# Optimization experiments

Measured on AMD Instinct MI355X. Metric: run time of the kernel, lower is better.

## Reference

```python
import jax, jax.numpy as jnp
import numpy as np

N_HEADS, D_K, D_MODEL = 16, 64, 1024
B, S = 2, 2048


def setup_inputs() -> dict:
    key = jax.random.key(0)
    ks = jax.random.split(key, 9)
    scale = 1.0 / np.sqrt(D_MODEL)
    cscale = 1.0 / np.sqrt(N_HEADS * D_K)
    return {
        "x": jax.random.normal(ks[0], (B, S, D_MODEL), dtype=jnp.float32),
        # per-head projection weights, stacked over heads: [H, d_model, d_k]
        "Wq": jax.random.uniform(ks[1], (N_HEADS, D_MODEL, D_K), jnp.float32, -scale, scale),
        "bq": jax.random.uniform(ks[2], (N_HEADS, D_K), jnp.float32, -scale, scale),
        "Wk": jax.random.uniform(ks[3], (N_HEADS, D_MODEL, D_K), jnp.float32, -scale, scale),
        "bk": jax.random.uniform(ks[4], (N_HEADS, D_K), jnp.float32, -scale, scale),
        "Wv": jax.random.uniform(ks[5], (N_HEADS, D_MODEL, D_K), jnp.float32, -scale, scale),
        "bv": jax.random.uniform(ks[6], (N_HEADS, D_K), jnp.float32, -scale, scale),
        # concat projection: [H*d_k, d_model]
        "Wc": jax.random.uniform(ks[7], (N_HEADS * D_K, D_MODEL), jnp.float32, -cscale, cscale),
        "bc": jax.random.uniform(ks[8], (D_MODEL,), jnp.float32, -cscale, cscale),
    }


def reference(x, Wq, bq, Wk, bk, Wv, bv, Wc, bc):
    # Per-head projections, vectorized across heads: [B,H,S,d_k]
    q = jnp.einsum("bsd,hdk->bhsk", x, Wq) + bq[None, :, None, :]
    k = jnp.einsum("bsd,hdk->bhsk", x, Wk) + bk[None, :, None, :]
    v = jnp.einsum("bsd,hdk->bhsk", x, Wv) + bv[None, :, None, :]
    # scores: [B,H,Sq,Skv]
    scores = jnp.einsum("bhsk,bhtk->bhst", q, k) / jnp.sqrt(jnp.asarray(D_K, x.dtype))
    # FAITHFUL to original: softmax over dim=1 of [B,S,S] = the QUERY axis (axis 2 here)
    attn = jax.nn.softmax(scores, axis=2)
    out = jnp.einsum("bhst,bhtk->bhsk", attn, v)  # [B,H,S,d_k]
    # concat heads along feature dim: [B,S,H*d_k]
    cat = jnp.transpose(out, (0, 2, 1, 3)).reshape(x.shape[0], x.shape[1], -1)
    return cat @ Wc + bc
```

## Files before the change

### kernel.cpp

```cpp
#include <hip/hip_runtime.h>

#define NH 16
#define DK 64
#define DM 1024
#define BB 2
#define SS 2048
#define BS (BB*SS)

typedef __attribute__((ext_vector_type(8))) short bf16x8;
typedef __attribute__((ext_vector_type(4))) short short4v;
typedef __attribute__((ext_vector_type(4))) float f32x4;

#define MFMA16 __builtin_amdgcn_mfma_f32_16x16x32_bf16

static __device__ __forceinline__ float bf2f(short s) {
  union { unsigned u; float f; } v;
  v.u = ((unsigned)(unsigned short)s) << 16;
  return v.f;
}
static __device__ __forceinline__ short f2bf(float f) {
  union { float f; unsigned u; } v; v.f = f;
  unsigned r = (v.u + 0x7fffu + ((v.u >> 16) & 1u)) >> 16;
  return (short)r;
}

template<int C16>
static __device__ __forceinline__ int soff(int row, int chunk) {
  return row*(C16*8) + ((chunk ^ (row & (C16-1))) << 3);
}

template<int C16, int R>
static __device__ __forceinline__ void stage(const short* __restrict__ g, int gstride,
                                             short* l, int wave, int lane) {
  const int rloc = lane / C16;
  const int c    = lane % C16;
#pragma unroll
  for (int rr = 0; rr < R; rr += 4*(64/C16)) {
    int rbase = rr + wave*(64/C16);
    int row   = rbase + rloc;
    int cg    = c ^ (row & (C16-1));
    __builtin_amdgcn_global_load_lds(
        (const __attribute__((address_space(1))) void*)(g + (size_t)row*gstride + cg*8),
        (__attribute__((address_space(3))) void*)(l + rbase*(C16*8)),
        16, 0, 0);
  }
}

__global__ __launch_bounds__(256) void k_convert(
    const float* __restrict__ x,
    const float* __restrict__ Wq, const float* __restrict__ Wk,
    const float* __restrict__ Wv, const float* __restrict__ Wc,
    short* __restrict__ xb, short* __restrict__ Wt, short* __restrict__ Wct) {
  __shared__ float T[64][65];
  const int tid = threadIdx.x;
  int bx = blockIdx.x;
  const int XB = BS*DM/(256*4);
  if (bx < XB) {
    int i = (bx*256 + tid)*4;
    float4 v = *(const float4*)&x[i];
    short4v o; o[0]=f2bf(v.x); o[1]=f2bf(v.y); o[2]=f2bf(v.z); o[3]=f2bf(v.w);
    *(short4v*)&xb[i] = o;
    return;
  }
  bx -= XB;
  if (bx < 48*16) {
    int th = bx >> 4, d0 = (bx & 15) * 64;
    int type = th >> 4, h = th & 15;
    const float* W = ((type == 0) ? Wq : (type == 1) ? Wk : Wv)
                     + (size_t)h*DM*DK + (size_t)d0*DK;
#pragma unroll
    for (int p = 0; p < 4; p++) {
      int dr = p*16 + (tid >> 4), dkc = (tid & 15) * 4;
      float4 v = *(const float4*)&W[(size_t)dr*DK + dkc];
      T[dkc+0][dr]=v.x; T[dkc+1][dr]=v.y; T[dkc+2][dr]=v.z; T[dkc+3][dr]=v.w;
    }
    __syncthreads();
#pragma unroll
    for (int e = 0; e < 2; e++) {
      int c = tid*2 + e, dk = c >> 3, dd = (c & 7) * 8;
      union { short s[8]; int4 v; } u;
#pragma unroll
      for (int j = 0; j < 8; j++) u.s[j] = f2bf(T[dk][dd+j]);
      *(int4*)&Wt[((size_t)th*DK + dk)*DM + d0 + dd] = u.v;
    }
    return;
  }
  bx -= 48*16;
  int n0 = (bx >> 4) * 64, k0 = (bx & 15) * 64;
#pragma unroll
  for (int p = 0; p < 4; p++) {
    int kr = p*16 + (tid >> 4), nc = (tid & 15) * 4;
    float4 v = *(const float4*)&Wc[(size_t)(k0+kr)*DM + n0 + nc];
    T[nc+0][kr]=v.x; T[nc+1][kr]=v.y; T[nc+2][kr]=v.z; T[nc+3][kr]=v.w;
  }
  __syncthreads();
#pragma unroll
  for (int e = 0; e < 2; e++) {
    int c = tid*2 + e, n = c >> 3, kk = (c & 7) * 8;
    union { short s[8]; int4 v; } u;
#pragma unroll
    for (int j = 0; j < 8; j++) u.s[j] = f2bf(T[n][kk+j]);
    *(int4*)&Wct[(size_t)(n0+n)*DM + k0 + kk] = u.v;
  }
}

__global__ __launch_bounds__(256) void k_qkv(
    const short* __restrict__ xb, const short* __restrict__ Wt,
    const float* __restrict__ bq, const float* __restrict__ bk,
    const float* __restrict__ bv,
    short* __restrict__ Qb, short* __restrict__ Kb, short* __restrict__ Vb) {
  __shared__ __align__(16) short As[128*64];
  __shared__ __align__(16) short Bs[128*64];
  const int tid = threadIdx.x, wave = tid >> 6, lane = tid & 63;
  const int l15 = lane & 15, quad = lane >> 4;
  const int m0 = blockIdx.x * 128, n0 = blockIdx.y * 128;
  const int mw = (wave & 1) * 64, nw = (wave >> 1) * 64;
  f32x4 acc[4][4] = {};
  for (int k0 = 0; k0 < DM; k0 += 64) {
    stage<8,128>(xb + (size_t)m0*DM + k0, DM, As, wave, lane);
    stage<8,128>(Wt + (size_t)n0*DM + k0, DM, Bs, wave, lane);
    __syncthreads();
#pragma unroll
    for (int ks = 0; ks < 2; ks++) {
      bf16x8 a[4], b[4];
#pragma unroll
      for (int g = 0; g < 4; g++)  a[g]  = *(const bf16x8*)&As[soff<8>(mw + g*16 + l15,  ks*4 + quad)];
#pragma unroll
      for (int nf = 0; nf < 4; nf++) b[nf] = *(const bf16x8*)&Bs[soff<8>(nw + nf*16 + l15, ks*4 + quad)];
#pragma unroll
      for (int g = 0; g < 4; g++)
#pragma unroll
        for (int nf = 0; nf < 4; nf++)
          acc[g][nf] = MFMA16(a[g], b[nf], acc[g][nf], 0, 0, 0);
    }
    __syncthreads();
  }
  const int th = (n0 + nw) >> 6;
  const int type = th >> 4, h = th & 15;
  short* dst = (type == 0) ? Qb : (type == 1) ? Kb : Vb;
  const float* bias = ((type == 0) ? bq : (type == 1) ? bk : bv) + h*DK;
  const float scale = (type == 0) ? 0.125f : 1.0f;
#pragma unroll
  for (int nf = 0; nf < 4; nf++) {
    int dk = nf*16 + l15;
    float bval = bias[dk];
#pragma unroll
    for (int g = 0; g < 4; g++)
#pragma unroll
      for (int r = 0; r < 4; r++) {
        int m = m0 + mw + g*16 + quad*4 + r;
        int b_ = m >> 11, s = m & (SS-1);
        dst[(size_t)((b_*NH + h)*SS + s)*DK + dk] = f2bf((acc[g][nf][r] + bval) * scale);
      }
  }
}

__global__ __launch_bounds__(256) void k_stats(
    const short* __restrict__ Qb, const short* __restrict__ Kb,
    const short* __restrict__ Vb, short* __restrict__ Vt) {
  __shared__ __align__(16) short Ks[128*64];
  __shared__ __align__(16) short Qs[128*64];
  __shared__ float red[4][64];
  __shared__ float zinv[128];
  const int tid = threadIdx.x, wave = tid >> 6, lane = tid & 63;
  const int l15 = lane & 15, quad = lane >> 4;
  const int t0 = blockIdx.x * 128;
  const int bh = blockIdx.y;
  const short* Qg = Qb + (size_t)bh * SS * DK;
  const short* Kg = Kb + (size_t)bh * SS * DK;
  const int mw = (wave & 1) * 64, nw = (wave >> 1) * 64;
  stage<8,128>(Kg + (size_t)t0*DK, DK, Ks, wave, lane);
  __syncthreads();
  bf16x8 kf[2][4];
#pragma unroll
  for (int ks = 0; ks < 2; ks++)
#pragma unroll
    for (int nf = 0; nf < 4; nf++)
      kf[ks][nf] = *(const bf16x8*)&Ks[soff<8>(nw + nf*16 + l15, ks*4 + quad)];
  float csum[4] = {0.f, 0.f, 0.f, 0.f};
  for (int s0 = 0; s0 < SS; s0 += 128) {
    stage<8,128>(Qg + (size_t)s0*DK, DK, Qs, wave, lane);
    __syncthreads();
    f32x4 acc[4][4] = {};
#pragma unroll
    for (int ks = 0; ks < 2; ks++) {
      bf16x8 a[4];
#pragma unroll
      for (int g = 0; g < 4; g++) a[g] = *(const bf16x8*)&Qs[soff<8>(mw + g*16 + l15, ks*4 + quad)];
#pragma unroll
      for (int g = 0; g < 4; g++)
#pragma unroll
        for (int nf = 0; nf < 4; nf++)
          acc[g][nf] = MFMA16(a[g], kf[ks][nf], acc[g][nf], 0, 0, 0);
    }
#pragma unroll
    for (int nf = 0; nf < 4; nf++)
#pragma unroll
      for (int g = 0; g < 4; g++)
#pragma unroll
        for (int r = 0; r < 4; r++)
          csum[nf] += __expf(acc[g][nf][r]);
    __syncthreads();
  }
#pragma unroll
  for (int nf = 0; nf < 4; nf++) {
    csum[nf] += __shfl_xor(csum[nf], 16, 64);
    csum[nf] += __shfl_xor(csum[nf], 32, 64);
  }
  if (lane < 16) {
#pragma unroll
    for (int nf = 0; nf < 4; nf++) red[wave][nf*16 + lane] = csum[nf];
  }
  __syncthreads();
  if (tid < 128) {
    int half = tid >> 6, c = tid & 63;
    zinv[tid] = 1.0f / (red[half*2][c] + red[half*2 + 1][c]);
  }
  __syncthreads();
  short* Vtile = Qs;
  const short* Vg = Vb + (size_t)bh * SS * DK;
#pragma unroll
  for (int it = 0; it < 4; it++) {
    int c = tid + it*256;
    int trow = c >> 3, c8 = (c & 7) * 8;
    union { int4 v; short s[8]; } u;
    u.v = *(const int4*)&Vg[(size_t)(t0 + trow)*DK + c8];
    float sc = zinv[trow];
#pragma unroll
    for (int j = 0; j < 8; j++) {
      int dk = c8 + j;
      Vtile[dk*128 + (((trow >> 3) ^ (dk & 15)) << 3) + (trow & 7)] = f2bf(bf2f(u.s[j]) * sc);
    }
  }
  __syncthreads();
  short* Vtg = Vt + (size_t)bh * DK * SS;
#pragma unroll
  for (int it = 0; it < 4; it++) {
    int row = it*16 + (tid >> 4), cc = tid & 15;
    *(int4*)&Vtg[(size_t)row*SS + t0 + cc*8] = *(const int4*)&Vtile[soff<16>(row, cc)];
  }
}

__global__ __launch_bounds__(256, 2) void k_attnpv(
    const short* __restrict__ Qb, const short* __restrict__ Kb,
    const short* __restrict__ Vt, short* __restrict__ catg) {
  __shared__ __align__(16) short Qs[128*64];
  __shared__ __align__(16) short Ks[128*64];
  __shared__ __align__(16) short Vs[64*128];
  __shared__ __align__(16) short Ps[128*128];
  const int tid = threadIdx.x, wave = tid >> 6, lane = tid & 63;
  const int l15 = lane & 15, quad = lane >> 4;
  const int s0 = blockIdx.x * 128;
  const int bh = blockIdx.y, b = bh >> 4, h = bh & 15;
  const short* Qg  = Qb + (size_t)bh * SS * DK;
  const short* Kg  = Kb + (size_t)bh * SS * DK;
  const short* Vtg = Vt + (size_t)bh * DK * SS;
  const int th_ = wave & 1, sh = wave >> 1;
  stage<8,128>(Qg + (size_t)s0*DK, DK, Qs, wave, lane);
  __syncthreads();
  bf16x8 qf[2][4];
#pragma unroll
  for (int ks = 0; ks < 2; ks++)
#pragma unroll
    for (int nf = 0; nf < 4; nf++)
      qf[ks][nf] = *(const bf16x8*)&Qs[soff<8>(sh*64 + nf*16 + l15, ks*4 + quad)];
  f32x4 out[4][4] = {};
  for (int t0 = 0; t0 < SS; t0 += 128) {
    stage<8,128>(Kg + (size_t)t0*DK, DK, Ks, wave, lane);
    stage<16,64>(Vtg + t0, SS, Vs, wave, lane);
    __syncthreads();
    f32x4 sacc[4][4] = {};
#pragma unroll
    for (int ks = 0; ks < 2; ks++) {
      bf16x8 a[4];
#pragma unroll
      for (int g = 0; g < 4; g++)
        a[g] = *(const bf16x8*)&Ks[soff<8>(th_*64 + g*16 + l15, ks*4 + quad)];
#pragma unroll
      for (int g = 0; g < 4; g++)
#pragma unroll
        for (int nf = 0; nf < 4; nf++)
          sacc[g][nf] = MFMA16(a[g], qf[ks][nf], sacc[g][nf], 0, 0, 0);
    }
#pragma unroll
    for (int g = 0; g < 4; g++)
#pragma unroll
      for (int nf = 0; nf < 4; nf++) {
        int s_loc = sh*64 + nf*16 + l15;
        int ct = th_*8 + g*2 + (quad >> 1);
        short4v p4;
        p4[0] = f2bf(__expf(sacc[g][nf][0]));
        p4[1] = f2bf(__expf(sacc[g][nf][1]));
        p4[2] = f2bf(__expf(sacc[g][nf][2]));
        p4[3] = f2bf(__expf(sacc[g][nf][3]));
        *(short4v*)&Ps[s_loc*128 + ((ct ^ (s_loc & 15)) << 3) + ((quad & 1) << 2)] = p4;
      }
    __syncthreads();
#pragma unroll
    for (int ks = 0; ks < 2; ks++) {
      bf16x8 pa[4], vb[4];
#pragma unroll
      for (int g = 0; g < 4; g++) {
        int s_loc = sh*64 + g*16 + l15;
        int ct2 = th_*8 + ks*4 + quad;
        pa[g] = *(const bf16x8*)&Ps[s_loc*128 + ((ct2 ^ (s_loc & 15)) << 3)];
      }
#pragma unroll
      for (int nf = 0; nf < 4; nf++)
        vb[nf] = *(const bf16x8*)&Vs[soff<16>(nf*16 + l15, th_*8 + ks*4 + quad)];
#pragma unroll
      for (int g = 0; g < 4; g++)
#pragma unroll
        for (int nf = 0; nf < 4; nf++)
          out[g][nf] = MFMA16(pa[g], vb[nf], out[g][nf], 0, 0, 0);
    }
    __syncthreads();
  }
  float* Pf = (float*)Ps;
  if (th_) {
#pragma unroll
    for (int g = 0; g < 4; g++)
#pragma unroll
      for (int nf = 0; nf < 4; nf++)
#pragma unroll
        for (int r = 0; r < 4; r++)
          Pf[sh*4096 + (g*16 + quad*4 + r)*64 + nf*16 + l15] = out[g][nf][r];
  }
  __syncthreads();
  if (!th_) {
#pragma unroll
    for (int g = 0; g < 4; g++)
#pragma unroll
      for (int nf = 0; nf < 4; nf++)
#pragma unroll
        for (int r = 0; r < 4; r++) {
          float v = out[g][nf][r] + Pf[sh*4096 + (g*16 + quad*4 + r)*64 + nf*16 + l15];
          int s = s0 + sh*64 + g*16 + quad*4 + r;
          catg[(size_t)(b*SS + s)*DM + h*DK + nf*16 + l15] = f2bf(v);
        }
  }
}

__global__ __launch_bounds__(256) void k_final(
    const short* __restrict__ catg, const short* __restrict__ Wct,
    const float* __restrict__ bc, float* __restrict__ out) {
  __shared__ __align__(16) short As[128*64];
  __shared__ __align__(16) short Bs[128*64];
  const int tid = threadIdx.x, wave = tid >> 6, lane = tid & 63;
  const int l15 = lane & 15, quad = lane >> 4;
  const int m0 = blockIdx.x * 128, n0 = blockIdx.y * 128;
  const int mw = (wave & 1) * 64, nw = (wave >> 1) * 64;
  f32x4 acc[4][4] = {};
  for (int k0 = 0; k0 < DM; k0 += 64) {
    stage<8,128>(catg + (size_t)m0*DM + k0, DM, As, wave, lane);
    stage<8,128>(Wct  + (size_t)n0*DM + k0, DM, Bs, wave, lane);
    __syncthreads();
#pragma unroll
    for (int ks = 0; ks < 2; ks++) {
      bf16x8 a[4], b[4];
#pragma unroll
      for (int g = 0; g < 4; g++)  a[g]  = *(const bf16x8*)&As[soff<8>(mw + g*16 + l15,  ks*4 + quad)];
#pragma unroll
      for (int nf = 0; nf < 4; nf++) b[nf] = *(const bf16x8*)&Bs[soff<8>(nw + nf*16 + l15, ks*4 + quad)];
#pragma unroll
      for (int g = 0; g < 4; g++)
#pragma unroll
        for (int nf = 0; nf < 4; nf++)
          acc[g][nf] = MFMA16(a[g], b[nf], acc[g][nf], 0, 0, 0);
    }
    __syncthreads();
  }
#pragma unroll
  for (int nf = 0; nf < 4; nf++) {
    int n = n0 + nw + nf*16 + l15;
    float bval = bc[n];
#pragma unroll
    for (int g = 0; g < 4; g++)
#pragma unroll
      for (int r = 0; r < 4; r++) {
        int m = m0 + mw + g*16 + quad*4 + r;
        out[(size_t)m*DM + n] = acc[g][nf][r] + bval;
      }
  }
}

extern "C" void kernel_launch(void* const* d_in, const int* in_sizes, int n_in,
                              void* d_out, int out_size, void* d_ws, size_t ws_size,
                              hipStream_t stream) {
  (void)in_sizes; (void)n_in; (void)out_size; (void)ws_size;
  const float* x  = (const float*)d_in[0];
  const float* Wq = (const float*)d_in[1];
  const float* bq = (const float*)d_in[2];
  const float* Wk = (const float*)d_in[3];
  const float* bk = (const float*)d_in[4];
  const float* Wv = (const float*)d_in[5];
  const float* bv = (const float*)d_in[6];
  const float* Wc = (const float*)d_in[7];
  const float* bc = (const float*)d_in[8];
  float* out = (float*)d_out;

  char* ws = (char*)d_ws;
  size_t o = 0;
  short* xb  = (short*)(ws + o); o += (size_t)BS*DM*2;
  short* Wt  = (short*)(ws + o); o += (size_t)3*NH*DK*DM*2;
  short* Wct = (short*)(ws + o); o += (size_t)DM*DM*2;
  short* Qb  = (short*)(ws + o); o += (size_t)BB*NH*SS*DK*2;
  short* Kb  = (short*)(ws + o); o += (size_t)BB*NH*SS*DK*2;
  short* Vb  = (short*)(ws + o); o += (size_t)BB*NH*SS*DK*2;
  short* Vt  = (short*)(ws + o); o += (size_t)BB*NH*DK*SS*2;
  short* cat = (short*)(ws + o); o += (size_t)BS*DM*2;

  const int nconv = BS*DM/(256*4) + 48*16 + 256;
  k_convert<<<dim3(nconv), 256, 0, stream>>>(x, Wq, Wk, Wv, Wc, xb, Wt, Wct);
  k_qkv   <<<dim3(BS/128, 3*NH*DK/128), 256, 0, stream>>>(xb, Wt, bq, bk, bv, Qb, Kb, Vb);
  k_stats <<<dim3(SS/128, BB*NH),       256, 0, stream>>>(Qb, Kb, Vb, Vt);
  k_attnpv<<<dim3(SS/128, BB*NH),       256, 0, stream>>>(Qb, Kb, Vt, cat);
  k_final <<<dim3(BS/128, DM/128),      256, 0, stream>>>(cat, Wct, bc, out);
}
```

Before: 239.5 us.

## Double-buffer Q/V tiles, remap blocks per XCD, use packed bf16 conversion

The stats and attention kernels now double-buffer their streamed Q and Vt tiles in shared memory. The next tile is prefetched while the current one computes, and one barrier per iteration is dropped in the stats loop. All GEMM and attention grids become 1D, with block indices remapped so that neighbouring tiles sharing a head or row band land on the same XCD, aiming for better L2 reuse. Bf16 packing switches to the library paired conversion intrinsic. Risks include races in the K buffer, which is refilled while other waves may still read it, and higher LDS use that lowers occupancy.

```diff
diff --git a/kernel.cpp b/kernel.cpp
--- a/kernel.cpp
+++ b/kernel.cpp
@@ -1,4 +1,5 @@
 #include <hip/hip_runtime.h>
+#include <hip/hip_bf16.h>
 
 #define NH 16
 #define DK 64
@@ -22,6 +23,10 @@
   union { float f; unsigned u; } v; v.f = f;
   unsigned r = (v.u + 0x7fffu + ((v.u >> 16) & 1u)) >> 16;
   return (short)r;
+}
+static __device__ __forceinline__ unsigned pkbf(float a, float b) {
+  __hip_bfloat162 h = __float22bfloat162_rn(make_float2(a, b));
+  union { __hip_bfloat162 h; unsigned u; } c; c.h = h; return c.u;
 }
 
 template<int C16>
@@ -58,8 +63,9 @@
   if (bx < XB) {
     int i = (bx*256 + tid)*4;
     float4 v = *(const float4*)&x[i];
-    short4v o; o[0]=f2bf(v.x); o[1]=f2bf(v.y); o[2]=f2bf(v.z); o[3]=f2bf(v.w);
-    *(short4v*)&xb[i] = o;
+    union { unsigned u[2]; short4v s; } o;
+    o.u[0] = pkbf(v.x, v.y); o.u[1] = pkbf(v.z, v.w);
+    *(short4v*)&xb[i] = o.s;
     return;
   }
   bx -= XB;
@@ -113,7 +119,8 @@
   __shared__ __align__(16) short Bs[128*64];
   const int tid = threadIdx.x, wave = tid >> 6, lane = tid & 63;
   const int l15 = lane & 15, quad = lane >> 4;
-  const int m0 = blockIdx.x * 128, n0 = blockIdx.y * 128;
+  const int id = blockIdx.x, xcd = id & 7, j = id >> 3;
+  const int m0 = (xcd*4 + (j & 3)) * 128, n0 = (j >> 2) * 128;
   const int mw = (wave & 1) * 64, nw = (wave >> 1) * 64;
   f32x4 acc[4][4] = {};
   for (int k0 = 0; k0 < DM; k0 += 64) {
@@ -158,18 +165,19 @@
 __global__ __launch_bounds__(256) void k_stats(
     const short* __restrict__ Qb, const short* __restrict__ Kb,
     const short* __restrict__ Vb, short* __restrict__ Vt) {
-  __shared__ __align__(16) short Ks[128*64];
-  __shared__ __align__(16) short Qs[128*64];
+  __shared__ __align__(16) short smem[3*8192];
   __shared__ float red[4][64];
   __shared__ float zinv[128];
+  short* Ks = smem;
   const int tid = threadIdx.x, wave = tid >> 6, lane = tid & 63;
   const int l15 = lane & 15, quad = lane >> 4;
-  const int t0 = blockIdx.x * 128;
-  const int bh = blockIdx.y;
+  const int id = blockIdx.x, xcd = id & 7, j = id >> 3;
+  const int bh = xcd*4 + (j & 3), t0 = (j >> 2) * 128;
   const short* Qg = Qb + (size_t)bh * SS * DK;
   const short* Kg = Kb + (size_t)bh * SS * DK;
   const int mw = (wave & 1) * 64, nw = (wave >> 1) * 64;
   stage<8,128>(Kg + (size_t)t0*DK, DK, Ks, wave, lane);
+  stage<8,128>(Qg, DK, smem + 8192, wave, lane);
   __syncthreads();
   bf16x8 kf[2][4];
 #pragma unroll
@@ -178,9 +186,11 @@
     for (int nf = 0; nf < 4; nf++)
       kf[ks][nf] = *(const bf16x8*)&Ks[soff<8>(nw + nf*16 + l15, ks*4 + quad)];
   float csum[4] = {0.f, 0.f, 0.f, 0.f};
-  for (int s0 = 0; s0 < SS; s0 += 128) {
-    stage<8,128>(Qg + (size_t)s0*DK, DK, Qs, wave, lane);
-    __syncthreads();
+  for (int it = 0; it < SS/128; it++) {
+    if (it + 1 < SS/128)
+      stage<8,128>(Qg + (size_t)(it+1)*128*DK, DK,
+                   smem + 8192 + (((it+1) & 1) << 13), wave, lane);
+    const short* Qs = smem + 8192 + ((it & 1) << 13);
     f32x4 acc[4][4] = {};
 #pragma unroll
     for (int ks = 0; ks < 2; ks++) {
@@ -217,7 +227,7 @@
     zinv[tid] = 1.0f / (red[half*2][c] + red[half*2 + 1][c]);
   }
   __syncthreads();
-  short* Vtile = Qs;
+  short* Vtile = smem + 8192;
   const short* Vg = Vb + (size_t)bh * SS * DK;
 #pragma unroll
   for (int it = 0; it < 4; it++) {
@@ -227,9 +237,9 @@
     u.v = *(const int4*)&Vg[(size_t)(t0 + trow)*DK + c8];
     float sc = zinv[trow];
 #pragma unroll
-    for (int j = 0; j < 8; j++) {
-      int dk = c8 + j;
-      Vtile[dk*128 + (((trow >> 3) ^ (dk & 15)) << 3) + (trow & 7)] = f2bf(bf2f(u.s[j]) * sc);
+    for (int jj = 0; jj < 8; jj++) {
+      int dk = c8 + jj;
+      Vtile[dk*128 + (((trow >> 3) ^ (dk & 15)) << 3) + (trow & 7)] = f2bf(bf2f(u.s[jj]) * sc);
     }
   }
   __syncthreads();
@@ -244,19 +254,22 @@
 __global__ __launch_bounds__(256, 2) void k_attnpv(
     const short* __restrict__ Qb, const short* __restrict__ Kb,
     const short* __restrict__ Vt, short* __restrict__ catg) {
-  __shared__ __align__(16) short Qs[128*64];
-  __shared__ __align__(16) short Ks[128*64];
-  __shared__ __align__(16) short Vs[64*128];
-  __shared__ __align__(16) short Ps[128*128];
+  __shared__ __align__(16) short smem[40960];
+  short* Qs = smem;
+  short* Ps = smem;
+  short* Ks = smem + 16384;
   const int tid = threadIdx.x, wave = tid >> 6, lane = tid & 63;
   const int l15 = lane & 15, quad = lane >> 4;
-  const int s0 = blockIdx.x * 128;
-  const int bh = blockIdx.y, b = bh >> 4, h = bh & 15;
+  const int id = blockIdx.x, xcd = id & 7, jj = id >> 3;
+  const int bh = xcd*4 + (jj & 3), s0 = (jj >> 2) * 128;
+  const int b = bh >> 4, h = bh & 15;
   const short* Qg  = Qb + (size_t)bh * SS * DK;
   const short* Kg  = Kb + (size_t)bh * SS * DK;
   const short* Vtg = Vt + (size_t)bh * DK * SS;
   const int th_ = wave & 1, sh = wave >> 1;
   stage<8,128>(Qg + (size_t)s0*DK, DK, Qs, wave, lane);
+  stage<8,128>(Kg, DK, Ks, wave, lane);
+  stage<16,64>(Vtg, SS, smem + 24576, wave, lane);
   __syncthreads();
   bf16x8 qf[2][4];
 #pragma unroll
@@ -264,11 +277,9 @@
 #pragma unroll
     for (int nf = 0; nf < 4; nf++)
       qf[ks][nf] = *(const bf16x8*)&Qs[soff<8>(sh*64 + nf*16 + l15, ks*4 + quad)];
+  __syncthreads();
   f32x4 out[4][4] = {};
-  for (int t0 = 0; t0 < SS; t0 += 128) {
-    stage<8,128>(Kg + (size_t)t0*DK, DK, Ks, wave, lane);
-    stage<16,64>(Vtg + t0, SS, Vs, wave, lane);
-    __syncthreads();
+  for (int it = 0; it < SS/128; it++) {
     f32x4 sacc[4][4] = {};
 #pragma unroll
     for (int ks = 0; ks < 2; ks++) {
@@ -288,14 +299,17 @@
       for (int nf = 0; nf < 4; nf++) {
         int s_loc = sh*64 + nf*16 + l15;
         int ct = th_*8 + g*2 + (quad >> 1);
-        short4v p4;
-        p4[0] = f2bf(__expf(sacc[g][nf][0]));
-        p4[1] = f2bf(__expf(sacc[g][nf][1]));
-        p4[2] = f2bf(__expf(sacc[g][nf][2]));
-        p4[3] = f2bf(__expf(sacc[g][nf][3]));
-        *(short4v*)&Ps[s_loc*128 + ((ct ^ (s_loc & 15)) << 3) + ((quad & 1) << 2)] = p4;
+        uint2 p;
+        p.x = pkbf(__expf(sacc[g][nf][0]), __expf(sacc[g][nf][1]));
+        p.y = pkbf(__expf(sacc[g][nf][2]), __expf(sacc[g][nf][3]));
+        *(uint2*)&Ps[s_loc*128 + ((ct ^ (s_loc & 15)) << 3) + ((quad & 1) << 2)] = p;
       }
     __syncthreads();
+    if (it + 1 < SS/128) {
+      stage<8,128>(Kg + (size_t)(it+1)*128*DK, DK, Ks, wave, lane);
+      stage<16,64>(Vtg + (it+1)*128, SS, smem + 24576 + (((it+1) & 1) << 13), wave, lane);
+    }
+    const short* Vs = smem + 24576 + ((it & 1) << 13);
 #pragma unroll
     for (int ks = 0; ks < 2; ks++) {
       bf16x8 pa[4], vb[4];
@@ -316,7 +330,7 @@
     }
     __syncthreads();
   }
-  float* Pf = (float*)Ps;
+  float* Pf = (float*)smem;
   if (th_) {
 #pragma unroll
     for (int g = 0; g < 4; g++)
@@ -348,7 +362,8 @@
   __shared__ __align__(16) short Bs[128*64];
   const int tid = threadIdx.x, wave = tid >> 6, lane = tid & 63;
   const int l15 = lane & 15, quad = lane >> 4;
-  const int m0 = blockIdx.x * 128, n0 = blockIdx.y * 128;
+  const int id = blockIdx.x, xcd = id & 7, j = id >> 3;
+  const int m0 = (xcd*4 + (j & 3)) * 128, n0 = (j >> 2) * 128;
   const int mw = (wave & 1) * 64, nw = (wave >> 1) * 64;
   f32x4 acc[4][4] = {};
   for (int k0 = 0; k0 < DM; k0 += 64) {
@@ -412,8 +427,8 @@
 
   const int nconv = BS*DM/(256*4) + 48*16 + 256;
   k_convert<<<dim3(nconv), 256, 0, stream>>>(x, Wq, Wk, Wv, Wc, xb, Wt, Wct);
-  k_qkv   <<<dim3(BS/128, 3*NH*DK/128), 256, 0, stream>>>(xb, Wt, bq, bk, bv, Qb, Kb, Vb);
-  k_stats <<<dim3(SS/128, BB*NH),       256, 0, stream>>>(Qb, Kb, Vb, Vt);
-  k_attnpv<<<dim3(SS/128, BB*NH),       256, 0, stream>>>(Qb, Kb, Vt, cat);
-  k_final <<<dim3(BS/128, DM/128),      256, 0, stream>>>(cat, Wct, bc, out);
-}
+  k_qkv   <<<dim3(768), 256, 0, stream>>>(xb, Wt, bq, bk, bv, Qb, Kb, Vb);
+  k_stats <<<dim3(512), 256, 0, stream>>>(Qb, Kb, Vb, Vt);
+  k_attnpv<<<dim3(512), 256, 0, stream>>>(Qb, Kb, Vt, cat);
+  k_final <<<dim3(256), 256, 0, stream>>>(cat, Wct, bc, out);
+}
```

Result: faster. 225.7 us (-5.8%).
